# Kernel tuning notes

Hardware: AMD Instinct MI355X
Metric: run time of the kernel (lower is better)

Reference implementation:

```python
import jax, jax.numpy as jnp
import numpy as np

LN_EPS = 1e-5  # torch nn.LayerNorm default
L2_EPS = 1e-12  # F.normalize default


def layer_norm(x, gamma, beta):
    mu = jnp.mean(x, axis=-1, keepdims=True)
    var = jnp.mean(jnp.square(x - mu), axis=-1, keepdims=True)
    return (x - mu) * jax.lax.rsqrt(var + LN_EPS) * gamma + beta


def l2_normalize(x):
    n = jnp.linalg.norm(x, axis=-1, keepdims=True)
    return x / jnp.maximum(n, L2_EPS)


def setup_inputs() -> dict:
    key = jax.random.key(0)
    k_x, k_mu = jax.random.split(key, 2)
    B, C, H, W = 4, 512, 128, 128
    K, M = 19, 5  # num_classes, num_components_per_class
    x = jax.random.normal(k_x, (B, C, H, W), dtype=jnp.float32)
    means = 0.02 * jax.random.normal(k_mu, (K, M, C), dtype=jnp.float32)  # trunc_normal_(std=0.02)
    diagonal = jnp.ones((K, M, C), dtype=jnp.float32)
    feat_gamma = jnp.ones((C,), dtype=jnp.float32)
    feat_beta = jnp.zeros((C,), dtype=jnp.float32)
    mask_gamma = jnp.ones((K,), dtype=jnp.float32)
    mask_beta = jnp.zeros((K,), dtype=jnp.float32)
    return dict(x=x, means=means, diagonal=diagonal,
                feat_gamma=feat_gamma, feat_beta=feat_beta,
                mask_gamma=mask_gamma, mask_beta=mask_beta)


def reference(x, means, diagonal, feat_gamma, feat_beta, mask_gamma, mask_beta):
    B, C, H, W = x.shape
    K, M, D = means.shape
    # rearrange 'b c h w -> (b h w) c'
    f = jnp.transpose(x, (0, 2, 3, 1)).reshape(-1, C)  # (N, D)
    f = layer_norm(f, feat_gamma, feat_beta)
    f = l2_normalize(f)
    # means are re-normalized in-place each forward
    mu = l2_normalize(means).reshape(K * M, D)          # (P, D), P = K*M
    sigma = diagonal.reshape(K * M, D)                  # diagonal scale (std)
    inv_var = 1.0 / jnp.square(sigma)
    # Mahalanobis distance via quadratic expansion (avoids (N,P,D) intermediate):
    # sum_d ((f - mu)/sigma)^2 = f^2 . iv - 2 f . (mu*iv) + sum(mu^2 * iv)
    q1 = jnp.square(f) @ inv_var.T                      # (N, P)
    q2 = f @ (mu * inv_var).T                           # (N, P)
    q3 = jnp.sum(jnp.square(mu) * inv_var, axis=-1)     # (P,)
    maha = q1 - 2.0 * q2 + q3[None, :]
    log_det = jnp.sum(jnp.log(sigma), axis=-1)          # sum log sigma, (P,)
    half_log2pi = 0.5 * D * jnp.log(2.0 * jnp.pi)
    log_prob = -0.5 * maha - log_det[None, :] - half_log2pi  # (N, P)
    log_prob = log_prob.reshape(-1, K, M)
    m_prob = jnp.max(log_prob, axis=-1)                 # amax over components, (N, K)
    out = layer_norm(m_prob, mask_gamma, mask_beta)
    # rearrange '(b h w) k -> b k h w'
    out_seg = jnp.transpose(out.reshape(B, H, W, K), (0, 3, 1, 2))
    return out_seg
```

## Files before the change

kernel.cpp:

```cpp
#include <hip/hip_runtime.h>
#include <math.h>

#define C_ 512
#define HW_ 16384
#define K_ 19
#define M_ 5
#define P_ 95
#define P2 96
#define TPX 32
#define NBLK 2048
#define HL2PI 470.49652900081467f

typedef __attribute__((ext_vector_type(8))) short short8;
typedef __attribute__((ext_vector_type(4))) int int4v;
typedef __attribute__((ext_vector_type(4))) float float4v;

static __device__ __forceinline__ short f2bf(float f) {
  unsigned u = __builtin_bit_cast(unsigned, f);
  unsigned r = (u + 0x7fffu + ((u >> 16) & 1u)) >> 16;
  return (short)r;
}
static __device__ __forceinline__ float bf2f(short s) {
  return __builtin_bit_cast(float, ((unsigned)(unsigned short)s) << 16);
}

static __device__ __forceinline__ int pk2(float a, float b) {
  int r;
  asm("v_cvt_pk_bf16_f32 %0, %1, %2" : "=v"(r) : "v"(a), "v"(b));
  return r;
}

static __device__ __forceinline__ short8 sq8(short8 a) {
  int4v ai = __builtin_bit_cast(int4v, a);
  int4v ri;
#pragma unroll
  for (int j = 0; j < 4; j++) {
    unsigned u = (unsigned)ai[j];
    float lo = __builtin_bit_cast(float, u << 16);
    float hi = __builtin_bit_cast(float, u & 0xffff0000u);
    ri[j] = pk2(lo * lo, hi * hi);
  }
  return __builtin_bit_cast(short8, ri);
}

__device__ __forceinline__ float block_reduce_sum(float v, volatile float* red) {
#pragma unroll
  for (int o = 32; o; o >>= 1) v += __shfl_down(v, o);
  const int lane = threadIdx.x & 63, wv = threadIdx.x >> 6;
  if (lane == 0) red[wv] = v;
  __syncthreads();
  float r = red[0] + red[1] + red[2] + red[3];
  __syncthreads();
  return r;
}

__global__ __launch_bounds__(256) void prep_kernel(
    const float* __restrict__ means, const float* __restrict__ diag,
    short* __restrict__ wbf, float* __restrict__ cterm) {
  const int p = blockIdx.x;
  const int tid = threadIdx.x;
  __shared__ float red[4];
  if (p >= P_) {
    for (int c = tid; c < C_; c += 256) {
      wbf[p * 1024 + c] = 0;
      wbf[p * 1024 + 512 + c] = 0;
    }
    if (tid == 0) cterm[p] = 0.f;
    return;
  }
  const float* mrow = means + (size_t)p * C_;
  const float* srow = diag + (size_t)p * C_;
  float m0 = mrow[tid], m1 = mrow[tid + 256];
  float ss = block_reduce_sum(m0 * m0 + m1 * m1, red);
  float rden = 1.f / fmaxf(sqrtf(ss), 1e-12f);
  float q3 = 0.f, ld = 0.f;
#pragma unroll
  for (int t = 0; t < 2; t++) {
    int c = tid + t * 256;
    float m = mrow[c], s = srow[c];
    float mu = m * rden;
    float iv = 1.f / (s * s);
    wbf[p * 1024 + c] = f2bf(iv);
    wbf[p * 1024 + 512 + c] = f2bf(mu * iv);
    q3 += mu * mu * iv;
    ld += logf(s);
  }
  q3 = block_reduce_sum(q3, red);
  ld = block_reduce_sum(ld, red);
  if (tid == 0) cterm[p] = -0.5f * q3 - ld - HL2PI;
}

__global__ __launch_bounds__(256) void main_kernel(
    const float* __restrict__ x,
    const float* __restrict__ fg, const float* __restrict__ fb,
    const float* __restrict__ mg, const float* __restrict__ mb,
    const short* __restrict__ wbf, const float* __restrict__ cterm,
    float* __restrict__ out) {
  __shared__ __align__(16) char raw[32768];
  __shared__ float redS[128], redQ[128];
  __shared__ float meanA[TPX], rstdA[TPX], rnA[TPX], rn2A[TPX];
  __shared__ float mean2A[TPX], rstd2A[TPX];
  __shared__ float mpr[TPX * 20];

  const int tid = threadIdx.x;
  const int wv = tid >> 6, lane = tid & 63;
  const int cg = tid >> 3, q = tid & 7;
  const int n0 = blockIdx.x * TPX;
  const int b = n0 >> 14;
  const int rem = n0 & 16383;
  const int h = rem >> 7;
  const int w0 = rem & 127;
  const int c16 = cg * 16;
  const int blkw = (q >> 2) * 16 + (cg >> 1);
  const int sbase = (q & 3) * 2 + (cg & 1);
  const float* xp4 = x + (size_t)b * C_ * HW_ + h * 128 + w0 + q * 4;

  float4v s4 = {0.f, 0.f, 0.f, 0.f}, q4 = {0.f, 0.f, 0.f, 0.f};
#pragma unroll
  for (int hc = 0; hc < 2; hc++) {
    float4v xq[8];
#pragma unroll
    for (int i = 0; i < 8; i++)
      xq[i] = *(const float4v*)(xp4 + (size_t)(c16 + hc * 8 + i) * HW_);
#pragma unroll
    for (int i = 0; i < 8; i++) {
      s4 += xq[i];
      q4 += xq[i] * xq[i];
    }
#pragma unroll
    for (int r = 0; r < 4; r++) {
      int4v pk;
#pragma unroll
      for (int j2 = 0; j2 < 4; j2++) pk[j2] = pk2(xq[2 * j2][r], xq[2 * j2 + 1][r]);
      *(int4v*)(raw + blkw * 1024 + ((hc * 4 + r) * 8 + sbase) * 16) = pk;
    }
  }
#pragma unroll
  for (int o = 8; o < 64; o <<= 1) {
#pragma unroll
    for (int c = 0; c < 4; c++) {
      s4[c] += __shfl_down(s4[c], o);
      q4[c] += __shfl_down(q4[c], o);
    }
  }
  if (lane < 8) {
    *(float4v*)(redS + (wv * 8 + lane) * 4) = s4;
    *(float4v*)(redQ + (wv * 8 + lane) * 4) = q4;
  }
  __syncthreads();
  if (tid < 32) {
    float ss = 0.f, qq = 0.f;
#pragma unroll
    for (int w = 0; w < 4; w++) {
      ss += redS[(w * 8 + (tid >> 2)) * 4 + (tid & 3)];
      qq += redQ[(w * 8 + (tid >> 2)) * 4 + (tid & 3)];
    }
    float mean = ss * (1.f / C_);
    float var = qq * (1.f / C_) - mean * mean;
    meanA[tid] = mean;
    rstdA[tid] = rsqrtf(var + 1e-5f);
  }
  __syncthreads();

  {
    float fga[16], fba[16];
#pragma unroll
    for (int i = 0; i < 4; i++) {
      *(float4v*)(fga + i * 4) = *(const float4v*)(fg + c16 + i * 4);
      *(float4v*)(fba + i * 4) = *(const float4v*)(fb + c16 + i * 4);
    }
    const float4v mean4 = *(const float4v*)(meanA + q * 4);
    const float4v rstd4 = *(const float4v*)(rstdA + q * 4);
    float4v s2 = {0.f, 0.f, 0.f, 0.f};
#pragma unroll
    for (int hc = 0; hc < 2; hc++) {
#pragma unroll
      for (int r = 0; r < 4; r++) {
        char* ad = raw + blkw * 1024 + ((hc * 4 + r) * 8 + sbase) * 16;
        short8 xc = *(short8*)ad;
        const float m = mean4[r], sd = rstd4[r];
        float vv[8];
#pragma unroll
        for (int j = 0; j < 8; j++) {
          float v = fmaf((bf2f(xc[j]) - m) * sd, fga[hc * 8 + j], fba[hc * 8 + j]);
          s2[r] = fmaf(v, v, s2[r]);
          vv[j] = v;
        }
        int4v pk;
#pragma unroll
        for (int j2 = 0; j2 < 4; j2++) pk[j2] = pk2(vv[2 * j2], vv[2 * j2 + 1]);
        *(int4v*)ad = pk;
      }
    }
#pragma unroll
    for (int o = 8; o < 64; o <<= 1) {
#pragma unroll
      for (int c = 0; c < 4; c++) s2[c] += __shfl_down(s2[c], o);
    }
    if (lane < 8) *(float4v*)(redS + (wv * 8 + lane) * 4) = s2;
  }
  __syncthreads();
  if (tid < 32) {
    float ss = 0.f;
#pragma unroll
    for (int w = 0; w < 4; w++) ss += redS[(w * 8 + (tid >> 2)) * 4 + (tid & 3)];
    float rn = 1.f / fmaxf(sqrtf(ss), 1e-12f);
    rnA[tid] = rn;
    rn2A[tid] = rn * rn;
  }
  __syncthreads();

  const int pbase = (wv & 1) * 3;
  const int khalf = wv >> 1;
  const int lm = lane & 15, lk = lane >> 4;
  const int slotR =
      ((((lane >> 4) & 1) * 4 + (lane & 3)) * 8 + ((lane >> 2) & 3) * 2 + ((lane >> 5) & 1)) * 16;
  float4v acc[3][2] = {{}, {}, {}};
  const short* wrow = wbf + (((pbase * 16 + lm) << 10) + (khalf << 9) + (lk << 3));
#pragma unroll 4
  for (int ksl = 0; ksl < 16; ksl++) {
    short8 a0 = *(const short8*)(wrow + ksl * 32);
    short8 a1 = *(const short8*)(wrow + 16384 + ksl * 32);
    short8 a2 = *(const short8*)(wrow + 32768 + ksl * 32);
    short8 b0 = *(const short8*)(raw + ksl * 1024 + slotR);
    short8 b1 = *(const short8*)(raw + (16 + ksl) * 1024 + slotR);
    if (khalf == 0) {
      b0 = sq8(b0);
      b1 = sq8(b1);
    }
    acc[0][0] = __builtin_amdgcn_mfma_f32_16x16x32_bf16(a0, b0, acc[0][0], 0, 0, 0);
    acc[0][1] = __builtin_amdgcn_mfma_f32_16x16x32_bf16(a0, b1, acc[0][1], 0, 0, 0);
    acc[1][0] = __builtin_amdgcn_mfma_f32_16x16x32_bf16(a1, b0, acc[1][0], 0, 0, 0);
    acc[1][1] = __builtin_amdgcn_mfma_f32_16x16x32_bf16(a1, b1, acc[1][1], 0, 0, 0);
    acc[2][0] = __builtin_amdgcn_mfma_f32_16x16x32_bf16(a2, b0, acc[2][0], 0, 0, 0);
    acc[2][1] = __builtin_amdgcn_mfma_f32_16x16x32_bf16(a2, b1, acc[2][1], 0, 0, 0);
  }
  __syncthreads();
  float* lp1 = (float*)raw;
  float* lp2 = (float*)(raw + 16384);

  if (khalf == 0) {
#pragma unroll
    for (int i = 0; i < 3; i++) {
      const int prow = (pbase + i) * 16 + lk * 4;
#pragma unroll
      for (int r = 0; r < 4; r++) {
        const float ct = cterm[prow + r];
#pragma unroll
        for (int t2 = 0; t2 < 2; t2++) {
          const int pxx = t2 * 16 + lm;
          lp1[pxx * 100 + prow + r] = fmaf(-0.5f * rn2A[pxx], acc[i][t2][r], ct);
        }
      }
    }
  } else {
#pragma unroll
    for (int i = 0; i < 3; i++) {
      const int prow = (pbase + i) * 16 + lk * 4;
#pragma unroll
      for (int r = 0; r < 4; r++) {
#pragma unroll
        for (int t2 = 0; t2 < 2; t2++) {
          const int pxx = t2 * 16 + lm;
          lp2[pxx * 100 + prow + r] = rnA[pxx] * acc[i][t2][r];
        }
      }
    }
  }
  __syncthreads();

  for (int idx = tid; idx < TPX * K_; idx += 256) {
    const int pxx = idx / K_;
    const int k = idx - pxx * K_;
    const float* r1 = lp1 + pxx * 100 + k * M_;
    const float* r2 = lp2 + pxx * 100 + k * M_;
    float mv = r1[0] + r2[0];
#pragma unroll
    for (int m = 1; m < M_; m++) mv = fmaxf(mv, r1[m] + r2[m]);
    mpr[pxx * 20 + k] = mv;
  }
  __syncthreads();
  if (tid < 32) {
    float ss = 0.f;
    for (int k = 0; k < K_; k++) ss += mpr[tid * 20 + k];
    float m2 = ss * (1.f / K_);
    float qq = 0.f;
    for (int k = 0; k < K_; k++) {
      float d = mpr[tid * 20 + k] - m2;
      qq += d * d;
    }
    mean2A[tid] = m2;
    rstd2A[tid] = rsqrtf(qq * (1.f / K_) + 1e-5f);
  }
  __syncthreads();
  float* obase = out + ((size_t)(b * K_) * 128 + h) * 128 + w0;
  for (int idx = tid; idx < TPX * K_; idx += 256) {
    const int k = idx >> 5, pxx = idx & 31;
    float v = fmaf((mpr[pxx * 20 + k] - mean2A[pxx]) * rstd2A[pxx], mg[k], mb[k]);
    obase[(size_t)k * HW_ + pxx] = v;
  }
}

extern "C" void kernel_launch(void* const* d_in, const int* in_sizes, int n_in,
                              void* d_out, int out_size, void* d_ws, size_t ws_size,
                              hipStream_t stream) {
  const float* x = (const float*)d_in[0];
  const float* means = (const float*)d_in[1];
  const float* diag = (const float*)d_in[2];
  const float* fg = (const float*)d_in[3];
  const float* fb = (const float*)d_in[4];
  const float* mg = (const float*)d_in[5];
  const float* mb = (const float*)d_in[6];
  float* out = (float*)d_out;

  short* wbf = (short*)d_ws;
  float* cterm = (float*)((char*)d_ws + (size_t)P2 * 1024 * 2);

  prep_kernel<<<P2, 256, 0, stream>>>(means, diag, wbf, cterm);
  main_kernel<<<NBLK, 256, 0, stream>>>(x, fg, fb, mg, mb, wbf, cterm, out);
}
```

Measured before the change: 69.38 us.

## Split per-pixel LayerNorm/L2 stats into separate pass with closed-form norm

Adds a stats kernel that reads x once and computes per-pixel mean, rstd and the L2 norm of the affine LayerNorm output in closed form, using gamma/beta moment sums prepared in the prep kernel. The main kernel then normalizes x directly before the bf16 pack. This removes the second LDS pass, two block reductions and the rn scaling in the epilogue. In exchange x (128 MB) is read twice from HBM, a third kernel launch is added, and the closed-form variance risks cancellation error.

```diff
diff --git a/kernel.cpp b/kernel.cpp
--- a/kernel.cpp
+++ b/kernel.cpp
@@ -20,9 +20,6 @@
   unsigned r = (u + 0x7fffu + ((u >> 16) & 1u)) >> 16;
   return (short)r;
 }
-static __device__ __forceinline__ float bf2f(short s) {
-  return __builtin_bit_cast(float, ((unsigned)(unsigned short)s) << 16);
-}
 
 static __device__ __forceinline__ int pk2(float a, float b) {
   int r;
@@ -56,7 +53,8 @@
 
 __global__ __launch_bounds__(256) void prep_kernel(
     const float* __restrict__ means, const float* __restrict__ diag,
-    short* __restrict__ wbf, float* __restrict__ cterm) {
+    const float* __restrict__ fg, const float* __restrict__ fb,
+    short* __restrict__ wbf, float* __restrict__ cterm, float* __restrict__ gsc) {
   const int p = blockIdx.x;
   const int tid = threadIdx.x;
   __shared__ float red[4];
@@ -65,7 +63,16 @@
       wbf[p * 1024 + c] = 0;
       wbf[p * 1024 + 512 + c] = 0;
     }
-    if (tid == 0) cterm[p] = 0.f;
+    float g0 = fg[tid], g1 = fg[tid + 256], b0 = fb[tid], b1 = fb[tid + 256];
+    float G1 = block_reduce_sum(g0 * b0 + g1 * b1, red);
+    float G2 = block_reduce_sum(g0 * g0 + g1 * g1, red);
+    float B2 = block_reduce_sum(b0 * b0 + b1 * b1, red);
+    if (tid == 0) {
+      cterm[p] = 0.f;
+      gsc[0] = G1;
+      gsc[1] = G2;
+      gsc[2] = B2;
+    }
     return;
   }
   const float* mrow = means + (size_t)p * C_;
@@ -90,15 +97,95 @@
   if (tid == 0) cterm[p] = -0.5f * q3 - ld - HL2PI;
 }
 
+__global__ __launch_bounds__(256) void stats_kernel(
+    const float* __restrict__ x, const float* __restrict__ fg,
+    const float* __restrict__ fb, const float* __restrict__ gsc,
+    float4v* __restrict__ pxs) {
+  __shared__ float red[5][128];
+  const int tid = threadIdx.x;
+  const int wv = tid >> 6, lane = tid & 63;
+  const int cg = tid >> 3, q = tid & 7;
+  const int c16 = cg * 16;
+  const int n0 = blockIdx.x * TPX;
+  const int b = n0 >> 14, rem = n0 & 16383, h = rem >> 7, w0 = rem & 127;
+  const float* xp4 = x + (size_t)b * C_ * HW_ + h * 128 + w0 + q * 4;
+
+  float ga[16], ba[16];
+#pragma unroll
+  for (int i = 0; i < 4; i++) {
+    *(float4v*)(ga + i * 4) = *(const float4v*)(fg + c16 + i * 4);
+    *(float4v*)(ba + i * 4) = *(const float4v*)(fb + c16 + i * 4);
+  }
+  float4v s1 = {0.f, 0.f, 0.f, 0.f}, s2 = s1, s3 = s1, s4 = s1, s5 = s1;
+#pragma unroll
+  for (int hc = 0; hc < 2; hc++) {
+    float4v xq[8];
+#pragma unroll
+    for (int i = 0; i < 8; i++)
+      xq[i] = *(const float4v*)(xp4 + (size_t)(c16 + hc * 8 + i) * HW_);
+#pragma unroll
+    for (int i = 0; i < 8; i++) {
+      const float g = ga[hc * 8 + i], bb = ba[hc * 8 + i];
+      const float gg = g * g, gb = g * bb;
+      float4v xx = xq[i] * xq[i];
+      s1 += xq[i];
+      s2 += xx;
+      s3 += gg * xq[i];
+      s4 += gg * xx;
+      s5 += gb * xq[i];
+    }
+  }
+#pragma unroll
+  for (int o = 8; o < 64; o <<= 1) {
+#pragma unroll
+    for (int c = 0; c < 4; c++) {
+      s1[c] += __shfl_down(s1[c], o);
+      s2[c] += __shfl_down(s2[c], o);
+      s3[c] += __shfl_down(s3[c], o);
+      s4[c] += __shfl_down(s4[c], o);
+      s5[c] += __shfl_down(s5[c], o);
+    }
+  }
+  if (lane < 8) {
+    *(float4v*)(&red[0][(wv * 8 + lane) * 4]) = s1;
+    *(float4v*)(&red[1][(wv * 8 + lane) * 4]) = s2;
+    *(float4v*)(&red[2][(wv * 8 + lane) * 4]) = s3;
+    *(float4v*)(&red[3][(wv * 8 + lane) * 4]) = s4;
+    *(float4v*)(&red[4][(wv * 8 + lane) * 4]) = s5;
+  }
+  __syncthreads();
+  if (tid < 32) {
+    float S[5] = {0.f, 0.f, 0.f, 0.f, 0.f};
+#pragma unroll
+    for (int w = 0; w < 4; w++) {
+      const int idx = (w * 8 + (tid >> 2)) * 4 + (tid & 3);
+#pragma unroll
+      for (int z = 0; z < 5; z++) S[z] += red[z][idx];
+    }
+    const float mean = S[0] * (1.f / C_);
+    const float var = S[1] * (1.f / C_) - mean * mean;
+    const float rstd = rsqrtf(var + 1e-5f);
+    const float G1 = gsc[0], G2 = gsc[1], B2 = gsc[2];
+    const float r2 = rstd * rstd;
+    float sv = r2 * S[3] + 2.f * rstd * S[4] - 2.f * mean * r2 * S[2] + B2 -
+               2.f * mean * rstd * G1 + mean * mean * r2 * G2;
+    const float rn = 1.f / fmaxf(sqrtf(fmaxf(sv, 0.f)), 1e-12f);
+    float4v o;
+    o[0] = mean;
+    o[1] = rn * rstd;
+    o[2] = rn;
+    o[3] = 0.f;
+    pxs[n0 + tid] = o;
+  }
+}
+
 __global__ __launch_bounds__(256) void main_kernel(
     const float* __restrict__ x,
     const float* __restrict__ fg, const float* __restrict__ fb,
     const float* __restrict__ mg, const float* __restrict__ mb,
     const short* __restrict__ wbf, const float* __restrict__ cterm,
-    float* __restrict__ out) {
+    const float4v* __restrict__ pxs, float* __restrict__ out) {
   __shared__ __align__(16) char raw[32768];
-  __shared__ float redS[128], redQ[128];
-  __shared__ float meanA[TPX], rstdA[TPX], rnA[TPX], rn2A[TPX];
   __shared__ float mean2A[TPX], rstd2A[TPX];
   __shared__ float mpr[TPX * 20];
 
@@ -115,7 +202,21 @@
   const int sbase = (q & 3) * 2 + (cg & 1);
   const float* xp4 = x + (size_t)b * C_ * HW_ + h * 128 + w0 + q * 4;
 
-  float4v s4 = {0.f, 0.f, 0.f, 0.f}, q4 = {0.f, 0.f, 0.f, 0.f};
+  float mu4[4], A4[4], rn4[4];
+#pragma unroll
+  for (int r = 0; r < 4; r++) {
+    float4v t = pxs[n0 + q * 4 + r];
+    mu4[r] = t[0];
+    A4[r] = t[1];
+    rn4[r] = t[2];
+  }
+  float ga[16], ba[16];
+#pragma unroll
+  for (int i = 0; i < 4; i++) {
+    *(float4v*)(ga + i * 4) = *(const float4v*)(fg + c16 + i * 4);
+    *(float4v*)(ba + i * 4) = *(const float4v*)(fb + c16 + i * 4);
+  }
+
 #pragma unroll
   for (int hc = 0; hc < 2; hc++) {
     float4v xq[8];
@@ -123,90 +224,17 @@
     for (int i = 0; i < 8; i++)
       xq[i] = *(const float4v*)(xp4 + (size_t)(c16 + hc * 8 + i) * HW_);
 #pragma unroll
-    for (int i = 0; i < 8; i++) {
-      s4 += xq[i];
-      q4 += xq[i] * xq[i];
-    }
-#pragma unroll
     for (int r = 0; r < 4; r++) {
+      const float mu = mu4[r], A = A4[r], rn = rn4[r];
+      float uu[8];
+#pragma unroll
+      for (int j = 0; j < 8; j++)
+        uu[j] = fmaf(ga[hc * 8 + j] * (xq[j][r] - mu), A, rn * ba[hc * 8 + j]);
       int4v pk;
 #pragma unroll
-      for (int j2 = 0; j2 < 4; j2++) pk[j2] = pk2(xq[2 * j2][r], xq[2 * j2 + 1][r]);
+      for (int j2 = 0; j2 < 4; j2++) pk[j2] = pk2(uu[2 * j2], uu[2 * j2 + 1]);
       *(int4v*)(raw + blkw * 1024 + ((hc * 4 + r) * 8 + sbase) * 16) = pk;
     }
-  }
-#pragma unroll
-  for (int o = 8; o < 64; o <<= 1) {
-#pragma unroll
-    for (int c = 0; c < 4; c++) {
-      s4[c] += __shfl_down(s4[c], o);
-      q4[c] += __shfl_down(q4[c], o);
-    }
-  }
-  if (lane < 8) {
-    *(float4v*)(redS + (wv * 8 + lane) * 4) = s4;
-    *(float4v*)(redQ + (wv * 8 + lane) * 4) = q4;
-  }
-  __syncthreads();
-  if (tid < 32) {
-    float ss = 0.f, qq = 0.f;
-#pragma unroll
-    for (int w = 0; w < 4; w++) {
-      ss += redS[(w * 8 + (tid >> 2)) * 4 + (tid & 3)];
-      qq += redQ[(w * 8 + (tid >> 2)) * 4 + (tid & 3)];
-    }
-    float mean = ss * (1.f / C_);
-    float var = qq * (1.f / C_) - mean * mean;
-    meanA[tid] = mean;
-    rstdA[tid] = rsqrtf(var + 1e-5f);
-  }
-  __syncthreads();
-
-  {
-    float fga[16], fba[16];
-#pragma unroll
-    for (int i = 0; i < 4; i++) {
-      *(float4v*)(fga + i * 4) = *(const float4v*)(fg + c16 + i * 4);
-      *(float4v*)(fba + i * 4) = *(const float4v*)(fb + c16 + i * 4);
-    }
-    const float4v mean4 = *(const float4v*)(meanA + q * 4);
-    const float4v rstd4 = *(const float4v*)(rstdA + q * 4);
-    float4v s2 = {0.f, 0.f, 0.f, 0.f};
-#pragma unroll
-    for (int hc = 0; hc < 2; hc++) {
-#pragma unroll
-      for (int r = 0; r < 4; r++) {
-        char* ad = raw + blkw * 1024 + ((hc * 4 + r) * 8 + sbase) * 16;
-        short8 xc = *(short8*)ad;
-        const float m = mean4[r], sd = rstd4[r];
-        float vv[8];
-#pragma unroll
-        for (int j = 0; j < 8; j++) {
-          float v = fmaf((bf2f(xc[j]) - m) * sd, fga[hc * 8 + j], fba[hc * 8 + j]);
-          s2[r] = fmaf(v, v, s2[r]);
-          vv[j] = v;
-        }
-        int4v pk;
-#pragma unroll
-        for (int j2 = 0; j2 < 4; j2++) pk[j2] = pk2(vv[2 * j2], vv[2 * j2 + 1]);
-        *(int4v*)ad = pk;
-      }
-    }
-#pragma unroll
-    for (int o = 8; o < 64; o <<= 1) {
-#pragma unroll
-      for (int c = 0; c < 4; c++) s2[c] += __shfl_down(s2[c], o);
-    }
-    if (lane < 8) *(float4v*)(redS + (wv * 8 + lane) * 4) = s2;
-  }
-  __syncthreads();
-  if (tid < 32) {
-    float ss = 0.f;
-#pragma unroll
-    for (int w = 0; w < 4; w++) ss += redS[(w * 8 + (tid >> 2)) * 4 + (tid & 3)];
-    float rn = 1.f / fmaxf(sqrtf(ss), 1e-12f);
-    rnA[tid] = rn;
-    rn2A[tid] = rn * rn;
   }
   __syncthreads();
 
@@ -249,7 +277,7 @@
 #pragma unroll
         for (int t2 = 0; t2 < 2; t2++) {
           const int pxx = t2 * 16 + lm;
-          lp1[pxx * 100 + prow + r] = fmaf(-0.5f * rn2A[pxx], acc[i][t2][r], ct);
+          lp1[pxx * 100 + prow + r] = fmaf(-0.5f, acc[i][t2][r], ct);
         }
       }
     }
@@ -262,7 +290,7 @@
 #pragma unroll
         for (int t2 = 0; t2 < 2; t2++) {
           const int pxx = t2 * 16 + lm;
-          lp2[pxx * 100 + prow + r] = rnA[pxx] * acc[i][t2][r];
+          lp2[pxx * 100 + prow + r] = acc[i][t2][r];
         }
       }
     }
@@ -314,8 +342,11 @@
   float* out = (float*)d_out;
 
   short* wbf = (short*)d_ws;
-  float* cterm = (float*)((char*)d_ws + (size_t)P2 * 1024 * 2);
-
-  prep_kernel<<<P2, 256, 0, stream>>>(means, diag, wbf, cterm);
-  main_kernel<<<NBLK, 256, 0, stream>>>(x, fg, fb, mg, mb, wbf, cterm, out);
-}
+  float* cterm = (float*)((char*)d_ws + 196608);
+  float* gsc = (float*)((char*)d_ws + 196608 + 384);
+  float4v* pxs = (float4v*)((char*)d_ws + 197120);
+
+  prep_kernel<<<P2, 256, 0, stream>>>(means, diag, fg, fb, wbf, cterm, gsc);
+  stats_kernel<<<NBLK, 256, 0, stream>>>(x, fg, fb, gsc, pxs);
+  main_kernel<<<NBLK, 256, 0, stream>>>(x, fg, fb, mg, mb, wbf, cterm, pxs, out);
+}
```

Result: slower. 98.35 us (+41.8%).
